# Kernel tuning notes

Hardware: AMD Instinct MI355X
Metric: run time of the kernel (lower is better)

Reference implementation:

```python
import jax, jax.numpy as jnp
import numpy as np
from jax import lax

B, CIN, COUT, H, W = 4, 256, 128, 64, 64
K, KK, PAD = 3, 9, 1
DK, DS, DP = 4, 2, 1  # deconv kernel/stride/pad
EPS = 1e-5


def setup_inputs() -> dict:
    key = jax.random.key(0)
    ks = jax.random.split(key, 6)
    x = jax.random.normal(ks[0], (B, CIN, H, W), jnp.float32)
    w_off = jax.random.normal(ks[1], (3 * KK, CIN, K, K), jnp.float32) * 0.01
    b_off = jnp.zeros((3 * KK,), jnp.float32)
    w_dcn = jax.random.normal(ks[2], (COUT, CIN, K, K), jnp.float32) / np.float32(np.sqrt(CIN * KK))
    b_dcn = jnp.zeros((COUT,), jnp.float32)
    gamma1 = jnp.ones((COUT,), jnp.float32)
    beta1 = jnp.zeros((COUT,), jnp.float32)
    # torch ConvTranspose2d weight layout: [in_ch, out_ch, kh, kw]
    w_up = jax.random.normal(ks[3], (COUT, COUT, DK, DK), jnp.float32) / np.float32(np.sqrt(COUT * DK * DK))
    gamma2 = jnp.ones((COUT,), jnp.float32)
    beta2 = jnp.zeros((COUT,), jnp.float32)
    return dict(x=x, w_off=w_off, b_off=b_off, w_dcn=w_dcn, b_dcn=b_dcn,
                gamma1=gamma1, beta1=beta1, w_up=w_up, gamma2=gamma2, beta2=beta2)


def _conv3(x, w, b):
    y = lax.conv_general_dilated(x, w, window_strides=(1, 1), padding=[(PAD, PAD), (PAD, PAD)],
                                 dimension_numbers=('NCHW', 'OIHW', 'NCHW'))
    return y + b[None, :, None, None]


def _bn(x, g, b):
    m = x.mean((0, 2, 3), keepdims=True)
    v = x.var((0, 2, 3), keepdims=True)
    return g[None, :, None, None] * (x - m) * lax.rsqrt(v + EPS) + b[None, :, None, None]


def _mdcn(x, offset, mask, w, b):
    # x: [B,C,H,W]; offset: [B,2*KK,H,W] interleaved (y,x) per kernel pt; mask: [B,KK,H,W]
    Bn, C, Hh, Ww = x.shape
    off = offset.reshape(Bn, KK, 2, Hh, Ww)
    dy, dx = off[:, :, 0], off[:, :, 1]                      # [B,KK,H,W]
    ky, kx = jnp.meshgrid(jnp.arange(K), jnp.arange(K), indexing='ij')
    ky = ky.reshape(KK).astype(x.dtype)
    kx = kx.reshape(KK).astype(x.dtype)
    ys = jnp.arange(Hh, dtype=x.dtype)[None, None, :, None] - PAD + ky[None, :, None, None] + dy
    xs = jnp.arange(Ww, dtype=x.dtype)[None, None, None, :] - PAD + kx[None, :, None, None] + dx
    y0f = jnp.floor(ys); x0f = jnp.floor(xs)
    ly = ys - y0f; lx = xs - x0f                              # fractional parts [B,KK,H,W]
    y0 = y0f.astype(jnp.int32); x0 = x0f.astype(jnp.int32)

    def gather(img, yi, xi):  # img [C,H,W], yi/xi [KK,H,W] -> [C,KK,H,W], zero out-of-bounds
        valid = ((yi >= 0) & (yi < Hh) & (xi >= 0) & (xi < Ww)).astype(img.dtype)
        v = img[:, jnp.clip(yi, 0, Hh - 1), jnp.clip(xi, 0, Ww - 1)]
        return v * valid[None]

    g = jax.vmap(gather)
    v00 = g(x, y0, x0)
    v01 = g(x, y0, x0 + 1)
    v10 = g(x, y0 + 1, x0)
    v11 = g(x, y0 + 1, x0 + 1)                                # [B,C,KK,H,W]
    val = (v00 * ((1 - ly) * (1 - lx))[:, None] + v01 * ((1 - ly) * lx)[:, None]
           + v10 * (ly * (1 - lx))[:, None] + v11 * (ly * lx)[:, None])
    val = val * mask[:, None]
    out = jnp.einsum('bckhw,ock->bohw', val, w.reshape(w.shape[0], C, KK))
    return out + b[None, :, None, None]


def _deconv(x, w_up):
    # torch ConvTranspose2d(k=DK, s=DS, p=DP) == fractionally strided conv with flipped kernel
    w = jnp.flip(jnp.transpose(w_up, (1, 0, 2, 3)), (2, 3))   # [out,in,kh,kw]
    p = DK - 1 - DP
    return lax.conv_general_dilated(x, w, window_strides=(1, 1), padding=[(p, p), (p, p)],
                                    lhs_dilation=(DS, DS), dimension_numbers=('NCHW', 'OIHW', 'NCHW'))


def reference(x, w_off, b_off, w_dcn, b_dcn, gamma1, beta1, w_up, gamma2, beta2):
    om = _conv3(x, w_off, b_off)                              # [B,27,H,W]
    o1, o2, m = jnp.split(om, 3, axis=1)
    offset = jnp.concatenate([o1, o2], axis=1)                # [B,18,H,W]
    mask = jax.nn.sigmoid(m)                                  # [B,9,H,W]
    y = _mdcn(x, offset, mask, w_dcn, b_dcn)                  # [B,COUT,H,W]
    y = jax.nn.relu(_bn(y, gamma1, beta1))
    y = _deconv(y, w_up)                                      # [B,COUT,2H,2W]
    y = jax.nn.relu(_bn(y, gamma2, beta2))
    return y
```

## Files before the change

### kernel.cpp

```cpp
#include <hip/hip_runtime.h>
#include <hip/hip_bf16.h>

typedef __attribute__((ext_vector_type(8))) short short8;
typedef __attribute__((ext_vector_type(4))) float f32x4;
typedef __attribute__((ext_vector_type(16))) float f32x16;
typedef unsigned short u16;
typedef unsigned int u32;

#define OFF_XT      0u
#define OFF_OM      8388608u
#define OFF_Y       10485760u
#define OFF_Y2      14680064u
#define OFF_BOFF    31457280u
#define OFF_BDCN    31604736u
#define OFF_BUP     32194560u
#define OFF_STATS   32718848u

__device__ __forceinline__ float lo2f(u32 u){ u32 v = u << 16; float f; __builtin_memcpy(&f, &v, 4); return f; }
__device__ __forceinline__ float hi2f(u32 u){ u32 v = u & 0xffff0000u; float f; __builtin_memcpy(&f, &v, 4); return f; }
__device__ __forceinline__ float b2f(u16 v){ u32 u = ((u32)v) << 16; float f; __builtin_memcpy(&f, &u, 4); return f; }
__device__ __forceinline__ u16 f2b(float f){ __hip_bfloat16 h = __float2bfloat16(f); u16 r; __builtin_memcpy(&r, &h, 2); return r; }
__device__ __forceinline__ u32 rne(float f){ u32 u; __builtin_memcpy(&u, &f, 4); return u + 0x7FFFu + ((u >> 16) & 1u); }
__device__ __forceinline__ u32 pk2(float f0, float f1){ return (rne(f0) >> 16) | (rne(f1) & 0xFFFF0000u); }

__device__ __forceinline__ f32x4 mfma16(short8 a, short8 b, f32x4 c){
  return __builtin_amdgcn_mfma_f32_16x16x32_bf16(a, b, c, 0, 0, 0);
}
__device__ __forceinline__ f32x16 mfma32(short8 a, short8 b, f32x16 c){
  return __builtin_amdgcn_mfma_f32_32x32x16_bf16(a, b, c, 0, 0, 0);
}
__device__ __forceinline__ void unpk(uint4 u, float* f){
  f[0]=lo2f(u.x); f[1]=hi2f(u.x); f[2]=lo2f(u.y); f[3]=hi2f(u.y);
  f[4]=lo2f(u.z); f[5]=hi2f(u.z); f[6]=lo2f(u.w); f[7]=hi2f(u.w);
}
__device__ __forceinline__ uint4 pk8(const float* f){
  uint4 r;
  r.x = pk2(f[0], f[1]); r.y = pk2(f[2], f[3]);
  r.z = pk2(f[4], f[5]); r.w = pk2(f[6], f[7]);
  return r;
}

__global__ __launch_bounds__(256) void prep_kernel(const float* __restrict__ w_off,
                                                   const float* __restrict__ w_dcn,
                                                   const float* __restrict__ w_up,
                                                   u16* __restrict__ Boff,
                                                   u16* __restrict__ Bdcn,
                                                   u16* __restrict__ Bup){
  int i = blockIdx.x * 256 + threadIdx.x;
  if (i < 72*2*64*8){
    int j = i & 7, lane = (i >> 3) & 63, nt = (i >> 9) & 1, kc = i >> 10;
    int n = nt*16 + (lane & 15);
    int k = kc*32 + ((lane >> 4) & 3)*8 + j, tap = k >> 8, c = k & 255;
    int ky = tap / 3, kx = tap - ky*3;
    u16 v = 0;
    if (n < 27) v = f2b(w_off[((n*256 + c)*3 + ky)*3 + kx]);
    Boff[i] = v;
  }
  if (i < 72*8*64*8){
    int j = i & 7, lane = (i >> 3) & 63, nt = (i >> 9) & 7, kc = i >> 12;
    int o = nt*16 + (lane & 15);
    int k = kc*32 + ((lane >> 4) & 3)*8 + j, tap = k >> 8, c = k & 255;
    int ky = tap / 3, kx = tap - ky*3;
    Bdcn[i] = f2b(w_dcn[((o*256 + c)*3 + ky)*3 + kx]);
  }
  if (i < 4*32*4*2*32*8){
    int j = i & 7, n = (i >> 3) & 31, kh = (i >> 8) & 1, a4 = (i >> 9) & 3;
    int kc = (i >> 11) & 31, pp = i >> 16;
    int k = kc*16 + kh*8 + j, tapd = k >> 7, c = k & 127;
    int o = a4*32 + n;
    int py = pp >> 1, px = pp & 1, dy = tapd >> 1, dx = tapd & 1;
    Bup[i] = f2b(w_up[((c*128 + o)*4 + (3-(py+2*dy)))*4 + (3-(px+2*dx))]);
  }
}

__global__ __launch_bounds__(256) void transpose_kernel(const float* __restrict__ x, u16* __restrict__ xt){
  __shared__ u16 Ls[64][65];
  int blk = blockIdx.x;
  int cb = blk & 3, h = (blk >> 2) & 63, b = blk >> 8;
  int t = threadIdx.x;
  int c0 = cb * 64;
  for (int i = 0; i < 16; i++){
    int idx = t + i*256;
    int c = idx >> 6, w = idx & 63;
    Ls[c][w] = f2b(x[((b*256 + c0 + c)*64 + h)*64 + w]);
  }
  __syncthreads();
  for (int i = 0; i < 16; i++){
    int idx = t + i*256;
    int w = idx >> 6, cc = idx & 63;
    xt[(((b*64 + h)*64 + w) << 8) + c0 + cc] = Ls[cc][w];
  }
}

__global__ __launch_bounds__(256, 8) void convoff_kernel(const u16* __restrict__ xt,
                                                         const u16* __restrict__ Boff,
                                                         const float* __restrict__ b_off,
                                                         float* __restrict__ om){
  __shared__ alignas(16) char smem[16896];
  u16* As0 = (u16*)smem;
  u16* As1 = (u16*)(smem + 8448);
  float* Ys = (float*)smem;
  int blk = blockIdx.x;
  int wt = blk & 3, h = (blk >> 2) & 63, b = blk >> 8;
  int w0 = wt * 16;
  int P0 = (b*64 + h)*64 + w0;
  int t = threadIdx.x;
  int wv = t >> 6, lane = t & 63;
  int ln = lane & 15, q4 = (lane >> 4) & 3;
  int spx = t >> 5, sc16a = t & 31;
  f32x4 acc[2];
  acc[0] = (f32x4){0.f,0.f,0.f,0.f};
  acc[1] = (f32x4){0.f,0.f,0.f,0.f};
  uint4 pf[2];

  {
    int ky = -1, kx = -1;
    #pragma unroll
    for (int it = 0; it < 2; it++){
      int px = spx + it*8;
      int y = h + ky, xw = w0 + px + kx;
      pf[it] = make_uint4(0,0,0,0);
      if ((u32)y < 64u && (u32)xw < 64u)
        pf[it] = *(const uint4*)(xt + (((b*64 + y)*64 + xw) << 8) + sc16a*8);
    }
    #pragma unroll
    for (int it = 0; it < 2; it++)
      *(uint4*)(As0 + (spx + it*8)*264 + sc16a*8) = pf[it];
  }
  __syncthreads();

  for (int tap = 0; tap < 9; tap++){
    const u16* cur = (tap & 1) ? As1 : As0;
    u16* nxt = (tap & 1) ? As0 : As1;
    if (tap < 8){
      int tn = tap + 1;
      int ky = tn/3 - 1, kx = tn - (tn/3)*3 - 1;
      #pragma unroll
      for (int it = 0; it < 2; it++){
        int px = spx + it*8;
        int y = h + ky, xw = w0 + px + kx;
        pf[it] = make_uint4(0,0,0,0);
        if ((u32)y < 64u && (u32)xw < 64u)
          pf[it] = *(const uint4*)(xt + (((b*64 + y)*64 + xw) << 8) + sc16a*8);
      }
    }
    #pragma unroll
    for (int q = 0; q < 2; q++){
      int kcl = wv*2 + q;
      int kcg = tap*8 + kcl;
      short8 a = *(const short8*)(cur + ln*264 + kcl*32 + q4*8);
      #pragma unroll
      for (int nt = 0; nt < 2; nt++){
        short8 bb = *(const short8*)(Boff + ((kcg*2 + nt)*64 + lane)*8);
        acc[nt] = mfma16(a, bb, acc[nt]);
      }
    }
    if (tap < 8){
      #pragma unroll
      for (int it = 0; it < 2; it++)
        *(uint4*)(nxt + (spx + it*8)*264 + sc16a*8) = pf[it];
    }
    __syncthreads();
  }
  #pragma unroll
  for (int nt = 0; nt < 2; nt++)
    #pragma unroll
    for (int r = 0; r < 4; r++)
      Ys[(wv*16 + q4*4 + r)*36 + nt*16 + ln] = acc[nt][r];
  __syncthreads();
  {
    int px = t >> 4, s = t & 15;
    #pragma unroll
    for (int half = 0; half < 2; half++){
      int n = s + half*16;
      if (n < 27){
        float sum = Ys[(px)*36 + n] + Ys[(16 + px)*36 + n]
                  + Ys[(32 + px)*36 + n] + Ys[(48 + px)*36 + n] + b_off[n];
        om[(P0 + px)*32 + n] = sum;
      }
    }
  }
}

__global__ __launch_bounds__(256, 4) void mdcn_kernel(const u16* __restrict__ xt,
                                                      const float* __restrict__ om,
                                                      const u16* __restrict__ Bdcn,
                                                      const float* __restrict__ b_dcn,
                                                      u16* __restrict__ yb){
  __shared__ alignas(16) char smem[21504];
  u16* As0 = (u16*)smem;
  u16* As1 = (u16*)(smem + 8448);
  float* Ptab = (float*)(smem + 16896);
  u16* Lp = (u16*)(smem + 8448);
  int blk = blockIdx.x;
  int wt = blk & 3, h = (blk >> 2) & 63, b = blk >> 8;
  int w0 = wt * 16;
  int P0 = (b*64 + h)*64 + w0;
  int t = threadIdx.x;
  int wv = t >> 6, lane = t & 63;
  int m = lane & 31, kh = lane >> 5;
  int ln = lane & 15, q4 = (lane >> 4) & 3;
  float bias0 = b_dcn[wv*32 + ln];
  float bias1 = b_dcn[wv*32 + 16 + ln];

  if (t < 144){
    int px = t / 9, tap = t - (t/9)*9;
    int ky = tap / 3, kx = tap - ky*3;
    const float* omp = om + (P0 + px)*32;
    float dy  = omp[2*tap];
    float dxv = omp[2*tap + 1];
    float mk  = 1.f / (1.f + __expf(-omp[18 + tap]));
    float ys = (float)(h - 1 + ky) + dy;
    float xs = (float)(w0 + px - 1 + kx) + dxv;
    float y0f = floorf(ys), x0f = floorf(xs);
    float ly = ys - y0f, lx = xs - x0f;
    int y0 = (int)y0f, x0 = (int)x0f;
    bool vy0 = (u32)y0 < 64u, vy1 = (u32)(y0+1) < 64u;
    bool vx0 = (u32)x0 < 64u, vx1 = (u32)(x0+1) < 64u;
    int ya = min(max(y0, 0), 63),   ybr_ = min(max(y0+1, 0), 63);
    int xa = min(max(x0, 0), 63),   xb = min(max(x0+1, 0), 63);
    u32 a00 = (u32)(((b*64 + ya)*64 + xa) << 8);
    u32 a01 = (u32)(((b*64 + ya)*64 + xb) << 8);
    u32 a10 = (u32)(((b*64 + ybr_)*64 + xa) << 8);
    u32 a11 = (u32)(((b*64 + ybr_)*64 + xb) << 8);
    float w00 = (vy0 && vx0) ? (1.f-ly)*(1.f-lx)*mk : 0.f;
    float w01 = (vy0 && vx1) ? (1.f-ly)*lx*mk       : 0.f;
    float w10 = (vy1 && vx0) ? ly*(1.f-lx)*mk       : 0.f;
    float w11 = (vy1 && vx1) ? ly*lx*mk             : 0.f;
    float* P = Ptab + t*8;
    ((u32*)P)[0] = a00; ((u32*)P)[1] = a01; ((u32*)P)[2] = a10; ((u32*)P)[3] = a11;
    P[4] = w00; P[5] = w01; P[6] = w10; P[7] = w11;
  }
  __syncthreads();

  f32x4 acc[2];
  acc[0] = (f32x4){0.f,0.f,0.f,0.f};
  acc[1] = (f32x4){0.f,0.f,0.f,0.f};
  uint4 pu[8];
  float4 pwv[2];

  auto prefetch = [&](int tap){
    #pragma unroll
    for (int i = 0; i < 2; i++){
      int p = wv*4 + i*2 + kh;
      const float* P = Ptab + (p*9 + tap)*8;
      uint4 pa = *(const uint4*)P;
      pwv[i] = *(const float4*)(P + 4);
      pu[i*4+0] = *(const uint4*)(xt + pa.x + m*8);
      pu[i*4+1] = *(const uint4*)(xt + pa.y + m*8);
      pu[i*4+2] = *(const uint4*)(xt + pa.z + m*8);
      pu[i*4+3] = *(const uint4*)(xt + pa.w + m*8);
    }
  };
  auto blend_write = [&](u16* dst){
    #pragma unroll
    for (int i = 0; i < 2; i++){
      int p = wv*4 + i*2 + kh;
      float f00[8], f01[8], f10[8], f11[8], s[8];
      unpk(pu[i*4+0], f00); unpk(pu[i*4+1], f01);
      unpk(pu[i*4+2], f10); unpk(pu[i*4+3], f11);
      float4 w = pwv[i];
      #pragma unroll
      for (int j = 0; j < 8; j++)
        s[j] = w.x*f00[j] + w.y*f01[j] + w.z*f10[j] + w.w*f11[j];
      *(uint4*)(dst + p*264 + m*8) = pk8(s);
    }
  };

  prefetch(0);
  blend_write(As0);
  __syncthreads();

  for (int tap = 0; tap < 9; tap++){
    const u16* cur = (tap & 1) ? As1 : As0;
    u16* nxt = (tap & 1) ? As0 : As1;
    if (tap < 8) prefetch(tap + 1);
    {
      int nt0 = wv*2, nt1 = wv*2 + 1;
      int kcg0 = tap*8;
      short8 b0n = *(const short8*)(Bdcn + ((kcg0*8 + nt0)*64 + lane)*8);
      short8 b1n = *(const short8*)(Bdcn + ((kcg0*8 + nt1)*64 + lane)*8);
      #pragma unroll
      for (int kc = 0; kc < 8; kc++){
        short8 b0 = b0n, b1 = b1n;
        if (kc < 7){
          int kcg = tap*8 + kc + 1;
          b0n = *(const short8*)(Bdcn + ((kcg*8 + nt0)*64 + lane)*8);
          b1n = *(const short8*)(Bdcn + ((kcg*8 + nt1)*64 + lane)*8);
        }
        short8 a = *(const short8*)(cur + ln*264 + kc*32 + q4*8);
        acc[0] = mfma16(a, b0, acc[0]);
        acc[1] = mfma16(a, b1, acc[1]);
      }
    }
    if (tap < 8) blend_write(nxt);
    __syncthreads();
  }
  #pragma unroll
  for (int nt2 = 0; nt2 < 2; nt2++){
    int ch = wv*32 + nt2*16 + ln;
    float bias = nt2 ? bias1 : bias0;
    #pragma unroll
    for (int r = 0; r < 4; r++){
      int px = q4*4 + r;
      Lp[px*136 + ch] = (u16)(rne(acc[nt2][r] + bias) >> 16);
    }
  }
  __syncthreads();
  {
    int px = t >> 4, cg = t & 15;
    uint4 u = *(const uint4*)(Lp + px*136 + cg*8);
    *(uint4*)(yb + (P0 + px)*128 + cg*8) = u;
  }
}

__global__ __launch_bounds__(256) void bnstats_kernel(const u16* __restrict__ src,
                                                      float* __restrict__ st, int npix){
  __shared__ float red[256];
  int t = threadIdx.x;
  int ch = t & 127, half = t >> 7;
  float s = 0.f, ss = 0.f;
  for (int p = blockIdx.x*2 + half; p < npix; p += gridDim.x*2){
    float v = b2f(src[p*128 + ch]);
    s += v; ss += v*v;
  }
  red[t] = s; __syncthreads();
  if (t < 128) atomicAdd(&st[t], red[t] + red[t+128]);
  __syncthreads();
  red[t] = ss; __syncthreads();
  if (t < 128) atomicAdd(&st[128 + t], red[t] + red[t+128]);
}

__global__ __launch_bounds__(256) void bnstats_nchw_kernel(const u16* __restrict__ y2n,
                                                           float* __restrict__ st){
  __shared__ float red[8];
  int ch = blockIdx.x;
  int t = threadIdx.x;
  int wv = t >> 6, lane = t & 63;
  float s = 0.f, ss = 0.f;
  for (int b = 0; b < 4; b++){
    const u16* base = y2n + (((b*128 + ch) << 14)) + t*8;
    #pragma unroll
    for (int it = 0; it < 8; it++){
      uint4 u = *(const uint4*)(base + it*2048);
      float f[8]; unpk(u, f);
      #pragma unroll
      for (int e = 0; e < 8; e++){ s += f[e]; ss += f[e]*f[e]; }
    }
  }
  #pragma unroll
  for (int o = 32; o >= 1; o >>= 1){
    s  += __shfl_xor(s, o);
    ss += __shfl_xor(ss, o);
  }
  if (lane == 0){ red[wv*2] = s; red[wv*2+1] = ss; }
  __syncthreads();
  if (t == 0) st[ch]       = red[0] + red[2] + red[4] + red[6];
  if (t == 1) st[128 + ch] = red[1] + red[3] + red[5] + red[7];
}

__global__ __launch_bounds__(256, 6) void deconv_kernel(const u16* __restrict__ yb,
                                                        const float* __restrict__ stats1,
                                                        const float* __restrict__ gamma1,
                                                        const float* __restrict__ beta1,
                                                        const u16* __restrict__ Bup,
                                                        u16* __restrict__ y2n){
  __shared__ alignas(16) char smem[19520];
  u16* Ls = (u16*)smem;
  u16* Lo = (u16*)smem;
  float2* bnL = (float2*)(smem + 18496);
  int blk = blockIdx.x;
  int half = blk & 1, yy = (blk >> 1) & 127, b = blk >> 8;
  int pary = yy & 1;
  int hs = (yy - 2 + pary) >> 1;
  int X0 = half * 64, wbase = half*32 - 1;
  int t = threadIdx.x;
  if (t < 128){
    float mean = stats1[t] * (1.f/16384.f);
    float var  = stats1[128 + t] * (1.f/16384.f) - mean*mean;
    float inv  = rsqrtf(var + 1e-5f);
    float sc   = gamma1[t] * inv;
    bnL[t] = make_float2(sc, beta1[t] - mean * sc);
  }
  __syncthreads();
  #pragma unroll
  for (int it = 0; it < 5; it++){
    int idx = it*256 + t;
    if (idx < 1088){
      int r = idx / 544, rem = idx - r*544;
      int cc = rem >> 4, c16 = rem & 15;
      int hh = hs + r, w_in = wbase + cc;
      uint4 u = make_uint4(0,0,0,0);
      if ((u32)hh < 64u && (u32)w_in < 64u)
        u = *(const uint4*)(yb + (((b*64 + hh)*64 + w_in) << 7) + c16*8);
      float f[8]; unpk(u, f);
      float o[8];
      #pragma unroll
      for (int e = 0; e < 8; e++){
        float2 sc = bnL[c16*8 + e];
        o[e] = fmaxf(0.f, fmaf(sc.x, f[e], sc.y));
      }
      *(uint4*)(Ls + (r*34 + cc)*136 + c16*8) = pk8(o);
    }
  }
  __syncthreads();

  int wv = t >> 6, lane = t & 63;
  int m = lane & 31, kh = lane >> 5;
  int parx = wv & 1, nh = wv >> 1;
  int pp = pary*2 + parx;
  f32x16 acc[2];
  acc[0] = (f32x16){0.f};
  acc[1] = (f32x16){0.f};

  #pragma unroll
  for (int tapd = 0; tapd < 4; tapd++){
    int dyy = tapd >> 1, dxx = tapd & 1;
    const u16* lp = Ls + ((dyy*34 + m + parx + dxx)*136);
    #pragma unroll
    for (int q = 0; q < 8; q++){
      short8 a = *(const short8*)(lp + q*16 + kh*8);
      #pragma unroll
      for (int nt2 = 0; nt2 < 2; nt2++){
        int a4 = nh*2 + nt2;
        short8 bb = *(const short8*)(Bup + ((((pp*32 + tapd*8 + q)*4 + a4)*2 + kh)*32 + m)*8);
        acc[nt2] = mfma32(a, bb, acc[nt2]);
      }
    }
  }
  __syncthreads();
  #pragma unroll
  for (int nt2 = 0; nt2 < 2; nt2++){
    int ch = (nh*2 + nt2)*32 + m;
    #pragma unroll
    for (int r = 0; r < 16; r++){
      int mrow = (r & 3) + 8*(r >> 2) + 4*kh;
      int xl = parx + 2*mrow;
      Lo[xl*136 + ch] = (u16)(rne(acc[nt2][r]) >> 16);
    }
  }
  __syncthreads();
  {
    int ch = t >> 1, xh = t & 1;
    u16* gp = y2n + ((b*128 + ch)*128 + yy)*128 + X0 + xh*32;
    #pragma unroll
    for (int g = 0; g < 4; g++){
      u32 r4[4];
      #pragma unroll
      for (int e = 0; e < 4; e++){
        u32 lo = Lo[(xh*32 + g*8 + 2*e)*136 + ch];
        u32 hi = Lo[(xh*32 + g*8 + 2*e + 1)*136 + ch];
        r4[e] = lo | (hi << 16);
      }
      *(uint4*)(gp + g*8) = make_uint4(r4[0], r4[1], r4[2], r4[3]);
    }
  }
}

__global__ __launch_bounds__(256) void final_kernel(const u16* __restrict__ y2n,
                                                    const float* __restrict__ stats2,
                                                    const float* __restrict__ gamma2,
                                                    const float* __restrict__ beta2,
                                                    float* __restrict__ outp){
  int gid = blockIdx.x*256 + threadIdx.x;
  int idx = gid * 8;
  int ch = (idx >> 14) & 127;
  float mean = stats2[ch] * (1.f/65536.f);
  float var  = stats2[128 + ch] * (1.f/65536.f) - mean*mean;
  float inv  = rsqrtf(var + 1e-5f);
  float scx  = gamma2[ch] * inv;
  float scy  = beta2[ch] - mean * scx;
  uint4 u = *(const uint4*)(y2n + idx);
  float f[8]; unpk(u, f);
  float4 o0, o1;
  o0.x = fmaxf(0.f, fmaf(scx, f[0], scy));
  o0.y = fmaxf(0.f, fmaf(scx, f[1], scy));
  o0.z = fmaxf(0.f, fmaf(scx, f[2], scy));
  o0.w = fmaxf(0.f, fmaf(scx, f[3], scy));
  o1.x = fmaxf(0.f, fmaf(scx, f[4], scy));
  o1.y = fmaxf(0.f, fmaf(scx, f[5], scy));
  o1.z = fmaxf(0.f, fmaf(scx, f[6], scy));
  o1.w = fmaxf(0.f, fmaf(scx, f[7], scy));
  *(float4*)(outp + idx)     = o0;
  *(float4*)(outp + idx + 4) = o1;
}

extern "C" void kernel_launch(void* const* d_in, const int* in_sizes, int n_in,
                              void* d_out, int out_size, void* d_ws, size_t ws_size,
                              hipStream_t stream) {
  const float* x      = (const float*)d_in[0];
  const float* w_off  = (const float*)d_in[1];
  const float* b_off  = (const float*)d_in[2];
  const float* w_dcn  = (const float*)d_in[3];
  const float* b_dcn  = (const float*)d_in[4];
  const float* gamma1 = (const float*)d_in[5];
  const float* beta1  = (const float*)d_in[6];
  const float* w_up   = (const float*)d_in[7];
  const float* gamma2 = (const float*)d_in[8];
  const float* beta2  = (const float*)d_in[9];

  char* ws = (char*)d_ws;
  u16*   xt    = (u16*)(ws + OFF_XT);
  float* om    = (float*)(ws + OFF_OM);
  u16*   yb    = (u16*)(ws + OFF_Y);
  u16*   y2n   = (u16*)(ws + OFF_Y2);
  u16*   Boff  = (u16*)(ws + OFF_BOFF);
  u16*   Bdcn  = (u16*)(ws + OFF_BDCN);
  u16*   Bup   = (u16*)(ws + OFF_BUP);
  float* stats = (float*)(ws + OFF_STATS);

  (void)hipMemsetAsync(stats, 0, 2048, stream);
  prep_kernel<<<1152, 256, 0, stream>>>(w_off, w_dcn, w_up, Boff, Bdcn, Bup);
  transpose_kernel<<<1024, 256, 0, stream>>>(x, xt);
  convoff_kernel<<<1024, 256, 0, stream>>>(xt, Boff, b_off, om);
  mdcn_kernel<<<1024, 256, 0, stream>>>(xt, om, Bdcn, b_dcn, yb);
  bnstats_kernel<<<256, 256, 0, stream>>>(yb, stats, 16384);
  deconv_kernel<<<1024, 256, 0, stream>>>(yb, stats, gamma1, beta1, Bup, y2n);
  bnstats_nchw_kernel<<<128, 256, 0, stream>>>(y2n, stats + 256);
  final_kernel<<<4096, 256, 0, stream>>>(y2n, stats + 256, gamma2, beta2, (float*)d_out);
}
```

Before: 191.9 us.

## Fuse BN statistics into producer epilogues and merge prep with transpose

Computes BatchNorm sum and sum-of-squares directly from the shared-memory output tiles in the mdcn and deconv epilogues, reducing per block and accumulating with atomics. This removes the two separate stats kernels that re-read the intermediates from global memory. It also merges weight prep and the input transpose into one launch. Together these cut three launches and two full passes over intermediate tensors, at the cost of many extra atomics, slightly more shared memory per block, and a nondeterministic summation order.

```diff
diff --git a/kernel.cpp b/kernel.cpp
--- a/kernel.cpp
+++ b/kernel.cpp
@@ -40,13 +40,34 @@
   return r;
 }
 
-__global__ __launch_bounds__(256) void prep_kernel(const float* __restrict__ w_off,
-                                                   const float* __restrict__ w_dcn,
-                                                   const float* __restrict__ w_up,
-                                                   u16* __restrict__ Boff,
-                                                   u16* __restrict__ Bdcn,
-                                                   u16* __restrict__ Bup){
-  int i = blockIdx.x * 256 + threadIdx.x;
+__global__ __launch_bounds__(256) void prep_transpose_kernel(const float* __restrict__ x,
+                                                             u16* __restrict__ xt,
+                                                             const float* __restrict__ w_off,
+                                                             const float* __restrict__ w_dcn,
+                                                             const float* __restrict__ w_up,
+                                                             u16* __restrict__ Boff,
+                                                             u16* __restrict__ Bdcn,
+                                                             u16* __restrict__ Bup){
+  __shared__ u16 Ls[64][65];
+  int blk = blockIdx.x;
+  int t = threadIdx.x;
+  if (blk < 1024){
+    int cb = blk & 3, h = (blk >> 2) & 63, b = blk >> 8;
+    int c0 = cb * 64;
+    for (int i = 0; i < 16; i++){
+      int idx = t + i*256;
+      int c = idx >> 6, w = idx & 63;
+      Ls[c][w] = f2b(x[((b*256 + c0 + c)*64 + h)*64 + w]);
+    }
+    __syncthreads();
+    for (int i = 0; i < 16; i++){
+      int idx = t + i*256;
+      int w = idx >> 6, cc = idx & 63;
+      xt[(((b*64 + h)*64 + w) << 8) + c0 + cc] = Ls[cc][w];
+    }
+    return;
+  }
+  int i = (blk - 1024) * 256 + t;
   if (i < 72*2*64*8){
     int j = i & 7, lane = (i >> 3) & 63, nt = (i >> 9) & 1, kc = i >> 10;
     int n = nt*16 + (lane & 15);
@@ -70,25 +91,6 @@
     int o = a4*32 + n;
     int py = pp >> 1, px = pp & 1, dy = tapd >> 1, dx = tapd & 1;
     Bup[i] = f2b(w_up[((c*128 + o)*4 + (3-(py+2*dy)))*4 + (3-(px+2*dx))]);
-  }
-}
-
-__global__ __launch_bounds__(256) void transpose_kernel(const float* __restrict__ x, u16* __restrict__ xt){
-  __shared__ u16 Ls[64][65];
-  int blk = blockIdx.x;
-  int cb = blk & 3, h = (blk >> 2) & 63, b = blk >> 8;
-  int t = threadIdx.x;
-  int c0 = cb * 64;
-  for (int i = 0; i < 16; i++){
-    int idx = t + i*256;
-    int c = idx >> 6, w = idx & 63;
-    Ls[c][w] = f2b(x[((b*256 + c0 + c)*64 + h)*64 + w]);
-  }
-  __syncthreads();
-  for (int i = 0; i < 16; i++){
-    int idx = t + i*256;
-    int w = idx >> 6, cc = idx & 63;
-    xt[(((b*64 + h)*64 + w) << 8) + c0 + cc] = Ls[cc][w];
   }
 }
 
@@ -186,12 +188,14 @@
                                                       const float* __restrict__ om,
                                                       const u16* __restrict__ Bdcn,
                                                       const float* __restrict__ b_dcn,
-                                                      u16* __restrict__ yb){
-  __shared__ alignas(16) char smem[21504];
+                                                      u16* __restrict__ yb,
+                                                      float* __restrict__ st1){
+  __shared__ alignas(16) char smem[22528];
   u16* As0 = (u16*)smem;
   u16* As1 = (u16*)(smem + 8448);
   float* Ptab = (float*)(smem + 16896);
   u16* Lp = (u16*)(smem + 8448);
+  float* red = (float*)(smem + 21504);
   int blk = blockIdx.x;
   int wt = blk & 3, h = (blk >> 2) & 63, b = blk >> 8;
   int w0 = wt * 16;
@@ -312,51 +316,22 @@
     uint4 u = *(const uint4*)(Lp + px*136 + cg*8);
     *(uint4*)(yb + (P0 + px)*128 + cg*8) = u;
   }
-}
-
-__global__ __launch_bounds__(256) void bnstats_kernel(const u16* __restrict__ src,
-                                                      float* __restrict__ st, int npix){
-  __shared__ float red[256];
-  int t = threadIdx.x;
-  int ch = t & 127, half = t >> 7;
-  float s = 0.f, ss = 0.f;
-  for (int p = blockIdx.x*2 + half; p < npix; p += gridDim.x*2){
-    float v = b2f(src[p*128 + ch]);
-    s += v; ss += v*v;
-  }
-  red[t] = s; __syncthreads();
-  if (t < 128) atomicAdd(&st[t], red[t] + red[t+128]);
-  __syncthreads();
-  red[t] = ss; __syncthreads();
-  if (t < 128) atomicAdd(&st[128 + t], red[t] + red[t+128]);
-}
-
-__global__ __launch_bounds__(256) void bnstats_nchw_kernel(const u16* __restrict__ y2n,
-                                                           float* __restrict__ st){
-  __shared__ float red[8];
-  int ch = blockIdx.x;
-  int t = threadIdx.x;
-  int wv = t >> 6, lane = t & 63;
-  float s = 0.f, ss = 0.f;
-  for (int b = 0; b < 4; b++){
-    const u16* base = y2n + (((b*128 + ch) << 14)) + t*8;
-    #pragma unroll
-    for (int it = 0; it < 8; it++){
-      uint4 u = *(const uint4*)(base + it*2048);
-      float f[8]; unpk(u, f);
-      #pragma unroll
-      for (int e = 0; e < 8; e++){ s += f[e]; ss += f[e]*f[e]; }
-    }
-  }
-  #pragma unroll
-  for (int o = 32; o >= 1; o >>= 1){
-    s  += __shfl_xor(s, o);
-    ss += __shfl_xor(ss, o);
-  }
-  if (lane == 0){ red[wv*2] = s; red[wv*2+1] = ss; }
-  __syncthreads();
-  if (t == 0) st[ch]       = red[0] + red[2] + red[4] + red[6];
-  if (t == 1) st[128 + ch] = red[1] + red[3] + red[5] + red[7];
+  {
+    int ch = t & 127, hf = t >> 7;
+    float s = 0.f, ss = 0.f;
+    #pragma unroll
+    for (int i = 0; i < 8; i++){
+      float v = b2f(Lp[(hf*8 + i)*136 + ch]);
+      s += v; ss += v*v;
+    }
+    red[t] = s;
+    __syncthreads();
+    if (t < 128) atomicAdd(&st1[t], red[t] + red[t+128]);
+    __syncthreads();
+    red[t] = ss;
+    __syncthreads();
+    if (t < 128) atomicAdd(&st1[128 + t], red[t] + red[t+128]);
+  }
 }
 
 __global__ __launch_bounds__(256, 6) void deconv_kernel(const u16* __restrict__ yb,
@@ -364,11 +339,13 @@
                                                         const float* __restrict__ gamma1,
                                                         const float* __restrict__ beta1,
                                                         const u16* __restrict__ Bup,
-                                                        u16* __restrict__ y2n){
-  __shared__ alignas(16) char smem[19520];
+                                                        u16* __restrict__ y2n,
+                                                        float* __restrict__ st2){
+  __shared__ alignas(16) char smem[20544];
   u16* Ls = (u16*)smem;
   u16* Lo = (u16*)smem;
   float2* bnL = (float2*)(smem + 18496);
+  float* red2 = (float*)(smem + 19520);
   int blk = blockIdx.x;
   int half = blk & 1, yy = (blk >> 1) & 127, b = blk >> 8;
   int pary = yy & 1;
@@ -454,6 +431,22 @@
       }
       *(uint4*)(gp + g*8) = make_uint4(r4[0], r4[1], r4[2], r4[3]);
     }
+  }
+  {
+    int ch = t & 127, hf = t >> 7;
+    float s = 0.f, ss = 0.f;
+    #pragma unroll
+    for (int i = 0; i < 32; i++){
+      float v = b2f(Lo[(hf*32 + i)*136 + ch]);
+      s += v; ss += v*v;
+    }
+    red2[t] = s;
+    __syncthreads();
+    if (t < 128) atomicAdd(&st2[t], red2[t] + red2[t+128]);
+    __syncthreads();
+    red2[t] = ss;
+    __syncthreads();
+    if (t < 128) atomicAdd(&st2[128 + t], red2[t] + red2[t+128]);
   }
 }
 
@@ -510,12 +503,9 @@
   float* stats = (float*)(ws + OFF_STATS);
 
   (void)hipMemsetAsync(stats, 0, 2048, stream);
-  prep_kernel<<<1152, 256, 0, stream>>>(w_off, w_dcn, w_up, Boff, Bdcn, Bup);
-  transpose_kernel<<<1024, 256, 0, stream>>>(x, xt);
+  prep_transpose_kernel<<<2176, 256, 0, stream>>>(x, xt, w_off, w_dcn, w_up, Boff, Bdcn, Bup);
   convoff_kernel<<<1024, 256, 0, stream>>>(xt, Boff, b_off, om);
-  mdcn_kernel<<<1024, 256, 0, stream>>>(xt, om, Bdcn, b_dcn, yb);
-  bnstats_kernel<<<256, 256, 0, stream>>>(yb, stats, 16384);
-  deconv_kernel<<<1024, 256, 0, stream>>>(yb, stats, gamma1, beta1, Bup, y2n);
-  bnstats_nchw_kernel<<<128, 256, 0, stream>>>(y2n, stats + 256);
+  mdcn_kernel<<<1024, 256, 0, stream>>>(xt, om, Bdcn, b_dcn, yb, stats);
+  deconv_kernel<<<1024, 256, 0, stream>>>(yb, stats, gamma1, beta1, Bup, y2n, stats + 256);
   final_kernel<<<4096, 256, 0, stream>>>(y2n, stats + 256, gamma2, beta2, (float*)d_out);
 }
```

Result: slower. 204.2 us (+6.4%).
